# Kernel optimization log

Hardware: AMD Instinct MI355X
Metric: run time of the kernel (lower is better)

Reference implementation:

```python
import jax, jax.numpy as jnp
import numpy as np


def _hann_filter(P):
    # ramp filter built in spatial domain (Kak & Slaney) times fftshifted Hann window
    n = np.concatenate([np.arange(1, P // 2 + 1, 2), np.arange(P // 2 - 1, 0, -2)]).astype(np.float64)
    f = np.zeros(P, np.float64)
    f[0] = 0.25
    f[1::2] = -1.0 / (np.pi * n) ** 2
    ramp = 2.0 * np.real(np.fft.fft(f))
    filt = ramp * np.fft.fftshift(np.hanning(P))
    return jnp.asarray(filt, jnp.float32)


def _fbp(sino, angles, circle):
    B, A, L = sino.shape
    P = max(64, int(2 ** np.ceil(np.log2(2 * L))))  # img_size_padded
    center = L // 2
    # --- FFT filtering (filtered=True) ---
    filt = _hann_filter(P)
    sino_p = jnp.pad(sino, ((0, 0), (0, 0), (0, P - L)))
    sino_f = jnp.real(jnp.fft.ifft(jnp.fft.fft(sino_p, axis=-1) * filt, axis=-1))[:, :, :L]
    # --- back-projection: emulate grid_sample(bilinear, align_corners=True, padding zeros) ---
    x, y = jnp.meshgrid(jnp.arange(L, dtype=jnp.float32) - center,
                        jnp.arange(L, dtype=jnp.float32) - center, indexing='ij')
    th = angles + jnp.pi / 2
    t = x[None] * jnp.cos(th)[:, None, None] + y[None] * jnp.sin(th)[:, None, None]  # [A,L,L]
    # t_norm = 2t/(L-1); align_corners pixel coord = (t_norm+1)/2*(L-1) = t + (L-1)/2
    u = t + (L - 1) / 2.0
    i0 = jnp.floor(u)
    frac = u - i0
    i0i = i0.astype(jnp.int32)
    i1i = i0i + 1
    v0 = (i0i >= 0) & (i0i < L)
    v1 = (i1i >= 0) & (i1i < L)
    w0 = jnp.where(v0, 1.0 - frac, 0.0)  # zero-padding: kill OOB taps
    w1 = jnp.where(v1, frac, 0.0)
    aidx = jnp.arange(A)[:, None, None]
    g0 = sino_f[:, aidx, jnp.clip(i0i, 0, L - 1)]  # [B,A,L,L]
    g1 = sino_f[:, aidx, jnp.clip(i1i, 0, L - 1)]
    recon = jnp.sum(w0[None] * g0 + w1[None] * g1, axis=1)  # [B,L,L]
    if circle:
        Y, X = np.ogrid[:L, :L]
        mask = jnp.asarray(np.sqrt((X - center) ** 2 + (Y - center) ** 2) > center)
        recon = jnp.where(mask[None], 0.0, recon)
    return recon


def setup_inputs() -> dict:
    key = jax.random.key(0)
    sino = jax.random.normal(key, (2, 181, 512), dtype=jnp.float32)
    angles = jnp.linspace(0.0, np.pi, 181).astype(jnp.float32)
    return {"sino": sino, "angles": angles, "circle": 1}


def reference(sino, angles, circle):
    return _fbp(sino, angles, circle)
```

## Files before the change

### kernel.cpp

```cpp
#include <hip/hip_runtime.h>
#include <math.h>

#define OFF_FILT 0
#define OFF_HR   1024
#define OFF_CTH  2048
#define OFF_STH  2304
#define OFF_SF   4096

__device__ __forceinline__ float cos2pi(float x) {
  return __builtin_amdgcn_cosf(x);
}

__global__ __launch_bounds__(256) void k_filt(const float* __restrict__ angles,
                                              float* __restrict__ ws,
                                              float* __restrict__ out) {
  const int t = threadIdx.x & 63;
  const int k = blockIdx.x * 4 + (threadIdx.x >> 6);
  float acc = 0.f;
#pragma unroll
  for (int q = 0; q < 8; q++) {
    int tt = t + 64 * q;
    int n = (tt < 256) ? (2 * tt + 1) : (1023 - 2 * tt);
    float pin = 3.14159265358979f * (float)n;
    float cf = -1.0f / (pin * pin);
    int r = ((2 * tt + 1) * k) & 1023;
    acc = fmaf(cf, cos2pi((float)r * (1.0f / 1024.0f)), acc);
  }
#pragma unroll
  for (int o = 32; o; o >>= 1) acc += __shfl_down(acc, o, 64);
  if (t == 0) {
    float ramp = 0.5f + 2.0f * acc;
    int ks = (k + 512) & 1023;
    float hann = 0.5f - 0.5f * cos2pi((float)ks * (1.0f / 1023.0f));
    ws[OFF_FILT + k] = ramp * hann;
  }
  if (blockIdx.x == 0 && threadIdx.x < 181) {
    float th = angles[threadIdx.x] + 1.5707963267948966f;
    ws[OFF_CTH + threadIdx.x] = cosf(th);
    ws[OFF_STH + threadIdx.x] = sinf(th);
  }
  const float4 z4 = make_float4(0.f, 0.f, 0.f, 0.f);
  float4* o4 = (float4*)out;
  int idx = blockIdx.x * 256 + threadIdx.x;
  o4[idx] = z4;
  o4[idx + 65536] = z4;
}

__global__ __launch_bounds__(256) void k_hr(float* __restrict__ ws) {
  const int t = threadIdx.x & 63;
  const int m = blockIdx.x * 4 + (threadIdx.x >> 6);
  float acc = 0.f;
  int r = (t * m) & 1023;
  const int step = (64 * m) & 1023;
#pragma unroll
  for (int q = 0; q < 16; q++) {
    acc = fmaf(ws[OFF_FILT + t + 64 * q],
               cos2pi((float)r * (1.0f / 1024.0f)), acc);
    r = (r + step) & 1023;
  }
#pragma unroll
  for (int o = 32; o; o >>= 1) acc += __shfl_down(acc, o, 64);
  if (t == 0) ws[OFF_HR + m] = acc * (1.0f / 1024.0f);
}

__global__ __launch_bounds__(64) void k_conv(const float* __restrict__ sino,
                                             float* __restrict__ ws) {
  __shared__ float s_s0[512];
  __shared__ float s_s1[512];
  __shared__ float s_hr[1024];
  const int t = threadIdx.x;
  const int a = blockIdx.x;
  const float4* r0 = (const float4*)(sino + (size_t)a * 512);
  const float4* r1 = (const float4*)(sino + (size_t)(181 + a) * 512);
  ((float4*)s_s0)[t] = r0[t];
  ((float4*)s_s0)[t + 64] = r0[t + 64];
  ((float4*)s_s1)[t] = r1[t];
  ((float4*)s_s1)[t + 64] = r1[t + 64];
  const float4* hr4 = (const float4*)(ws + OFF_HR);
#pragma unroll
  for (int q = 0; q < 4; q++) ((float4*)s_hr)[t + 64 * q] = hr4[t + 64 * q];
  __syncthreads();

  const int base = blockIdx.y * 256 + t * 4;
  float acc0[4] = {0.f, 0.f, 0.f, 0.f};
  float acc1[4] = {0.f, 0.f, 0.f, 0.f};
  const float4* SH = (const float4*)s_hr;
  const float4* S0 = (const float4*)s_s0;
  const float4* S1 = (const float4*)s_s1;
  for (int j8 = 0; j8 < 512; j8 += 8) {
    float4 sa0 = S0[j8 >> 2];
    float4 sb0 = S0[(j8 >> 2) + 1];
    float4 sa1 = S1[j8 >> 2];
    float4 sb1 = S1[(j8 >> 2) + 1];
    int w = base - j8;
    float4 h0 = SH[((w - 8) & 1023) >> 2];
    float4 h1 = SH[((w - 4) & 1023) >> 2];
    float4 h2 = SH[(w & 1023) >> 2];
    float qq[12] = {h0.x, h0.y, h0.z, h0.w, h1.x, h1.y,
                    h1.z, h1.w, h2.x, h2.y, h2.z, h2.w};
    float v0[8] = {sa0.x, sa0.y, sa0.z, sa0.w, sb0.x, sb0.y, sb0.z, sb0.w};
    float v1[8] = {sa1.x, sa1.y, sa1.z, sa1.w, sb1.x, sb1.y, sb1.z, sb1.w};
#pragma unroll
    for (int jj = 0; jj < 8; jj++) {
#pragma unroll
      for (int m = 0; m < 4; m++) {
        acc0[m] = fmaf(v0[jj], qq[8 + m - jj], acc0[m]);
        acc1[m] = fmaf(v1[jj], qq[8 + m - jj], acc1[m]);
      }
    }
  }
  float* dst = ws + OFF_SF + (size_t)a * 1024 + base * 2;
  ((float4*)dst)[0] = make_float4(acc0[0], acc1[0], acc0[1], acc1[1]);
  ((float4*)dst)[1] = make_float4(acc0[2], acc1[2], acc0[3], acc1[3]);
}

#define PAD   108
#define ROWE  728
#define CHUNK 4
__global__ __launch_bounds__(512) void k_bp(const float* __restrict__ ws,
                                            const int* __restrict__ circ,
                                            float* __restrict__ out) {
  __shared__ float2 srow[CHUNK * ROWE];
  const int j = threadIdx.x;
  const int i = blockIdx.x;
  const int abase = blockIdx.y * 91;
  const int acnt = min(91, 181 - abase);
  const float xc = (float)(i - 256);
  const float yc = (float)(j - 256);
  const float* __restrict__ cth = ws + OFF_CTH;
  const float* __restrict__ sth = ws + OFF_STH;
  float acc0 = 0.f, acc1 = 0.f;

  const float2 z2 = make_float2(0.f, 0.f);
#pragma unroll
  for (int r = 0; r < CHUNK; r++) {
    if (j < PAD) srow[r * ROWE + j] = z2;
    if (j < ROWE - PAD - 512) srow[r * ROWE + PAD + 512 + j] = z2;
  }

  const int r0 = j >> 8, r1 = r0 + 2;
  const int p0 = (j & 255) * 2;
  const int col = j & 255;
  const float4* __restrict__ G = (const float4*)(ws + OFF_SF);
  float4* SW0 = (float4*)&srow[r0 * ROWE + PAD + p0];
  float4* SW1 = (float4*)&srow[r1 * ROWE + PAD + p0];
  const int rowcap = abase + acnt - 1;

  int A = abase;
  float4 pre0 = G[min(A + r0, rowcap) * 256 + col];
  float4 pre1 = G[min(A + r1, rowcap) * 256 + col];

  for (int c = 0; c < 23; c++) {
    __syncthreads();
    *SW0 = pre0;
    *SW1 = pre1;
    const int An = A + CHUNK;
    if (c < 22) {
      pre0 = G[min(An + r0, rowcap) * 256 + col];
      pre1 = G[min(An + r1, rowcap) * 256 + col];
    }
    __syncthreads();
    const int nv = min(CHUNK, abase + acnt - A);
#pragma unroll
    for (int r = 0; r < CHUNK; r++) {
      if (r >= nv) break;
      const int a = A + r;
      const float c_ = cth[a];
      const float s_ = sth[a];
      float u = fmaf(xc, c_, fmaf(yc, s_, 255.5f + (float)PAD));
      float fl = floorf(u);
      float fr = u - fl;
      int b = (int)fl;
      const float2* rp = &srow[r * ROWE];
      float2 t0 = rp[b];
      float2 t1 = rp[b + 1];
      float w0 = 1.0f - fr;
      acc0 = fmaf(w0, t0.x, fmaf(fr, t1.x, acc0));
      acc1 = fmaf(w0, t0.y, fmaf(fr, t1.y, acc1));
    }
    A = An;
  }
  const int dx = j - 256, dy = i - 256;
  const bool msk = (circ[0] != 0) && (dx * dx + dy * dy > 65536);
  if (!msk) {
    const size_t o = (size_t)i * 512 + j;
    atomicAdd(&out[o], acc0);
    atomicAdd(&out[262144 + o], acc1);
  }
}

extern "C" void kernel_launch(void* const* d_in, const int* in_sizes, int n_in,
                              void* d_out, int out_size, void* d_ws, size_t ws_size,
                              hipStream_t stream) {
  const float* sino = (const float*)d_in[0];
  const float* angles = (const float*)d_in[1];
  const int* circ = (const int*)d_in[2];
  float* ws = (float*)d_ws;
  float* out = (float*)d_out;

  hipLaunchKernelGGL(k_filt, dim3(256),    dim3(256), 0, stream, angles, ws, out);
  hipLaunchKernelGGL(k_hr,   dim3(256),    dim3(256), 0, stream, ws);
  hipLaunchKernelGGL(k_conv, dim3(181, 2), dim3(64),  0, stream, sino, ws);
  hipLaunchKernelGGL(k_bp,   dim3(512, 2), dim3(512), 0, stream, ws, circ, out);
}
```

Baseline: 96.53 us.

## Fuse all FBP stages into one cooperative persistent kernel with grid syncs

Replaces the four separate launches (filter build, impulse response, convolution, back-projection) with a single cooperative kernel of 512 blocks that separates the phases with grid.sync(). The convolution is split across 8 wavefronts per block with a shared-memory reduction. The back-projection now processes all 181 angles per row block, so the output is written directly and no longer zeroed and accumulated with atomics. This removes launch gaps and atomics, but it relies on all 512 blocks being co-resident, pays for grid-wide barriers, and halves the number of back-projection blocks. The old four-kernel path is kept as a fallback if the cooperative launch fails.

```diff
diff --git a/kernel.cpp b/kernel.cpp
--- a/kernel.cpp
+++ b/kernel.cpp
@@ -1,5 +1,8 @@
 #include <hip/hip_runtime.h>
+#include <hip/hip_cooperative_groups.h>
 #include <math.h>
+
+namespace cg = cooperative_groups;
 
 #define OFF_FILT 0
 #define OFF_HR   1024
@@ -7,8 +10,194 @@
 #define OFF_STH  2304
 #define OFF_SF   4096
 
+#define PAD   108
+#define ROWE  728
+#define CHUNK 4
+
 __device__ __forceinline__ float cos2pi(float x) {
   return __builtin_amdgcn_cosf(x);
+}
+
+__global__ __launch_bounds__(512, 4) void k_fused(const float* __restrict__ sino,
+                                                  const float* __restrict__ angles,
+                                                  const int* __restrict__ circ,
+                                                  float* __restrict__ ws,
+                                                  float* __restrict__ out) {
+  cg::grid_group grid = cg::this_grid();
+  __shared__ float smem[6144];
+  const int tid = threadIdx.x;
+  const int bid = blockIdx.x;
+  const int lane = tid & 63;
+
+  if (tid < 128) {
+    const int k = bid * 2 + (tid >> 6);
+    float acc = 0.f;
+#pragma unroll
+    for (int q = 0; q < 8; q++) {
+      int tt = lane + 64 * q;
+      int n = (tt < 256) ? (2 * tt + 1) : (1023 - 2 * tt);
+      float pin = 3.14159265358979f * (float)n;
+      float cf = -1.0f / (pin * pin);
+      int r = ((2 * tt + 1) * k) & 1023;
+      acc = fmaf(cf, cos2pi((float)r * (1.0f / 1024.0f)), acc);
+    }
+#pragma unroll
+    for (int o = 32; o; o >>= 1) acc += __shfl_down(acc, o, 64);
+    if (lane == 0) {
+      float ramp = 0.5f + 2.0f * acc;
+      int ks = (k + 512) & 1023;
+      float hann = 0.5f - 0.5f * cos2pi((float)ks * (1.0f / 1023.0f));
+      ws[OFF_FILT + k] = ramp * hann;
+    }
+  } else if (bid == 0 && tid < 309) {
+    int a = tid - 128;
+    float th = angles[a] + 1.5707963267948966f;
+    ws[OFF_CTH + a] = cosf(th);
+    ws[OFF_STH + a] = sinf(th);
+  }
+  grid.sync();
+
+  if (tid < 128) {
+    const int m = bid * 2 + (tid >> 6);
+    float acc = 0.f;
+    int r = (lane * m) & 1023;
+    const int step = (64 * m) & 1023;
+#pragma unroll
+    for (int q = 0; q < 16; q++) {
+      acc = fmaf(ws[OFF_FILT + lane + 64 * q],
+                 cos2pi((float)r * (1.0f / 1024.0f)), acc);
+      r = (r + step) & 1023;
+    }
+#pragma unroll
+    for (int o = 32; o; o >>= 1) acc += __shfl_down(acc, o, 64);
+    if (lane == 0) ws[OFF_HR + m] = acc * (1.0f / 1024.0f);
+  }
+  grid.sync();
+
+  if (bid < 362) {
+    const int a = bid >> 1;
+    const int half = bid & 1;
+    float* s_s0 = smem;
+    float* s_s1 = smem + 512;
+    float* s_hr = smem + 1024;
+    float* part = smem + 2048;
+    if (tid < 128) {
+      ((float4*)s_s0)[tid] = ((const float4*)(sino + (size_t)a * 512))[tid];
+    } else if (tid < 256) {
+      ((float4*)s_s1)[tid - 128] =
+          ((const float4*)(sino + (size_t)(181 + a) * 512))[tid - 128];
+    } else {
+      ((float4*)s_hr)[tid - 256] = ((const float4*)(ws + OFF_HR))[tid - 256];
+    }
+    __syncthreads();
+
+    const int w = tid >> 6;
+    const int base = half * 256 + lane * 4;
+    float acc0[4] = {0.f, 0.f, 0.f, 0.f};
+    float acc1[4] = {0.f, 0.f, 0.f, 0.f};
+    const float4* SH = (const float4*)s_hr;
+    const float4* S0 = (const float4*)s_s0;
+    const float4* S1 = (const float4*)s_s1;
+#pragma unroll
+    for (int ii = 0; ii < 8; ii++) {
+      const int j8 = w * 64 + ii * 8;
+      float4 sa0 = S0[j8 >> 2];
+      float4 sb0 = S0[(j8 >> 2) + 1];
+      float4 sa1 = S1[j8 >> 2];
+      float4 sb1 = S1[(j8 >> 2) + 1];
+      int wi = base - j8;
+      float4 h0 = SH[((wi - 8) & 1023) >> 2];
+      float4 h1 = SH[((wi - 4) & 1023) >> 2];
+      float4 h2 = SH[(wi & 1023) >> 2];
+      float qq[12] = {h0.x, h0.y, h0.z, h0.w, h1.x, h1.y,
+                      h1.z, h1.w, h2.x, h2.y, h2.z, h2.w};
+      float v0[8] = {sa0.x, sa0.y, sa0.z, sa0.w, sb0.x, sb0.y, sb0.z, sb0.w};
+      float v1[8] = {sa1.x, sa1.y, sa1.z, sa1.w, sb1.x, sb1.y, sb1.z, sb1.w};
+#pragma unroll
+      for (int jj = 0; jj < 8; jj++) {
+#pragma unroll
+        for (int m = 0; m < 4; m++) {
+          acc0[m] = fmaf(v0[jj], qq[8 + m - jj], acc0[m]);
+          acc1[m] = fmaf(v1[jj], qq[8 + m - jj], acc1[m]);
+        }
+      }
+    }
+    float* pw = part + w * 512 + lane * 8;
+    ((float4*)pw)[0] = make_float4(acc0[0], acc1[0], acc0[1], acc1[1]);
+    ((float4*)pw)[1] = make_float4(acc0[2], acc1[2], acc0[3], acc1[3]);
+    __syncthreads();
+    float s = part[tid];
+#pragma unroll
+    for (int ww = 1; ww < 8; ww++) s += part[ww * 512 + tid];
+    ws[OFF_SF + (size_t)a * 1024 + half * 512 + tid] = s;
+  }
+  grid.sync();
+
+  {
+    float2* srow = (float2*)smem;
+    const int j = tid;
+    const int i = bid;
+    const float xc = (float)(i - 256);
+    const float yc = (float)(j - 256);
+    const float* __restrict__ cth = ws + OFF_CTH;
+    const float* __restrict__ sth = ws + OFF_STH;
+    float acc0 = 0.f, acc1 = 0.f;
+
+    const float2 z2 = make_float2(0.f, 0.f);
+#pragma unroll
+    for (int r = 0; r < CHUNK; r++) {
+      if (j < PAD) srow[r * ROWE + j] = z2;
+      if (j < ROWE - PAD - 512) srow[r * ROWE + PAD + 512 + j] = z2;
+    }
+
+    const int r0 = j >> 8, r1 = r0 + 2;
+    const int p0 = (j & 255) * 2;
+    const int col = j & 255;
+    const float4* __restrict__ G = (const float4*)(ws + OFF_SF);
+    float4* SW0 = (float4*)&srow[r0 * ROWE + PAD + p0];
+    float4* SW1 = (float4*)&srow[r1 * ROWE + PAD + p0];
+    const int rowcap = 180;
+
+    int A = 0;
+    float4 pre0 = G[min(r0, rowcap) * 256 + col];
+    float4 pre1 = G[min(r1, rowcap) * 256 + col];
+
+    for (int c = 0; c < 46; c++) {
+      __syncthreads();
+      *SW0 = pre0;
+      *SW1 = pre1;
+      const int An = A + CHUNK;
+      if (c < 45) {
+        pre0 = G[min(An + r0, rowcap) * 256 + col];
+        pre1 = G[min(An + r1, rowcap) * 256 + col];
+      }
+      __syncthreads();
+      const int nv = min(CHUNK, 181 - A);
+#pragma unroll
+      for (int r = 0; r < CHUNK; r++) {
+        if (r >= nv) break;
+        const int a = A + r;
+        const float c_ = cth[a];
+        const float s_ = sth[a];
+        float u = fmaf(xc, c_, fmaf(yc, s_, 255.5f + (float)PAD));
+        float fl = floorf(u);
+        float fr = u - fl;
+        int b = (int)fl;
+        const float2* rp = &srow[r * ROWE];
+        float2 t0 = rp[b];
+        float2 t1 = rp[b + 1];
+        float w0 = 1.0f - fr;
+        acc0 = fmaf(w0, t0.x, fmaf(fr, t1.x, acc0));
+        acc1 = fmaf(w0, t0.y, fmaf(fr, t1.y, acc1));
+      }
+      A = An;
+    }
+    const int dx = j - 256, dy = i - 256;
+    const bool msk = (circ[0] != 0) && (dx * dx + dy * dy > 65536);
+    const size_t o = (size_t)i * 512 + j;
+    out[o] = msk ? 0.f : acc0;
+    out[262144 + o] = msk ? 0.f : acc1;
+  }
 }
 
 __global__ __launch_bounds__(256) void k_filt(const float* __restrict__ angles,
@@ -114,9 +303,6 @@
   ((float4*)dst)[1] = make_float4(acc0[2], acc1[2], acc0[3], acc1[3]);
 }
 
-#define PAD   108
-#define ROWE  728
-#define CHUNK 4
 __global__ __launch_bounds__(512) void k_bp(const float* __restrict__ ws,
                                             const int* __restrict__ circ,
                                             float* __restrict__ out) {
@@ -198,8 +384,14 @@
   float* ws = (float*)d_ws;
   float* out = (float*)d_out;
 
-  hipLaunchKernelGGL(k_filt, dim3(256),    dim3(256), 0, stream, angles, ws, out);
-  hipLaunchKernelGGL(k_hr,   dim3(256),    dim3(256), 0, stream, ws);
-  hipLaunchKernelGGL(k_conv, dim3(181, 2), dim3(64),  0, stream, sino, ws);
-  hipLaunchKernelGGL(k_bp,   dim3(512, 2), dim3(512), 0, stream, ws, circ, out);
-}
+  void* args[] = {(void*)&sino, (void*)&angles, (void*)&circ, (void*)&ws, (void*)&out};
+  hipError_t e = hipLaunchCooperativeKernel(reinterpret_cast<void*>(k_fused),
+                                            dim3(512), dim3(512), args, 0, stream);
+  if (e != hipSuccess) {
+    (void)hipGetLastError();
+    hipLaunchKernelGGL(k_filt, dim3(256),    dim3(256), 0, stream, angles, ws, out);
+    hipLaunchKernelGGL(k_hr,   dim3(256),    dim3(256), 0, stream, ws);
+    hipLaunchKernelGGL(k_conv, dim3(181, 2), dim3(64),  0, stream, sino, ws);
+    hipLaunchKernelGGL(k_bp,   dim3(512, 2), dim3(512), 0, stream, ws, circ, out);
+  }
+}
```

After: 259.8 us. +169.1%, slower.

## Split convolution across 8 waves and drop angle split with atomics in backprojection

Applied to the files above, without the earlier changes.

The convolution kernel now uses 512 threads per block, with each wave handling a 64-sample slice of the input and partial sums reduced through shared memory. This raises parallelism over the previous single-wave blocks. The backprojection no longer splits angles across two blocks. Each block loops over all 181 angles and writes its output directly, so the output zeroing pass and the atomic adds are removed. The catch is half as many backprojection blocks, each with twice the serial work, plus a cheaper truncation in place of floor, which relies on the coordinate being non-negative thanks to the padding.

```diff
diff --git a/kernel.cpp b/kernel.cpp
--- a/kernel.cpp
+++ b/kernel.cpp
@@ -7,13 +7,16 @@
 #define OFF_STH  2304
 #define OFF_SF   4096
 
+#define PAD   108
+#define ROWE  728
+#define CHUNK 4
+
 __device__ __forceinline__ float cos2pi(float x) {
   return __builtin_amdgcn_cosf(x);
 }
 
 __global__ __launch_bounds__(256) void k_filt(const float* __restrict__ angles,
-                                              float* __restrict__ ws,
-                                              float* __restrict__ out) {
+                                              float* __restrict__ ws) {
   const int t = threadIdx.x & 63;
   const int k = blockIdx.x * 4 + (threadIdx.x >> 6);
   float acc = 0.f;
@@ -39,11 +42,6 @@
     ws[OFF_CTH + threadIdx.x] = cosf(th);
     ws[OFF_STH + threadIdx.x] = sinf(th);
   }
-  const float4 z4 = make_float4(0.f, 0.f, 0.f, 0.f);
-  float4* o4 = (float4*)out;
-  int idx = blockIdx.x * 256 + threadIdx.x;
-  o4[idx] = z4;
-  o4[idx + 65536] = z4;
 }
 
 __global__ __launch_bounds__(256) void k_hr(float* __restrict__ ws) {
@@ -63,39 +61,45 @@
   if (t == 0) ws[OFF_HR + m] = acc * (1.0f / 1024.0f);
 }
 
-__global__ __launch_bounds__(64) void k_conv(const float* __restrict__ sino,
-                                             float* __restrict__ ws) {
-  __shared__ float s_s0[512];
-  __shared__ float s_s1[512];
-  __shared__ float s_hr[1024];
-  const int t = threadIdx.x;
-  const int a = blockIdx.x;
-  const float4* r0 = (const float4*)(sino + (size_t)a * 512);
-  const float4* r1 = (const float4*)(sino + (size_t)(181 + a) * 512);
-  ((float4*)s_s0)[t] = r0[t];
-  ((float4*)s_s0)[t + 64] = r0[t + 64];
-  ((float4*)s_s1)[t] = r1[t];
-  ((float4*)s_s1)[t + 64] = r1[t + 64];
-  const float4* hr4 = (const float4*)(ws + OFF_HR);
-#pragma unroll
-  for (int q = 0; q < 4; q++) ((float4*)s_hr)[t + 64 * q] = hr4[t + 64 * q];
+__global__ __launch_bounds__(512) void k_conv(const float* __restrict__ sino,
+                                              float* __restrict__ ws) {
+  __shared__ float smem[6144];
+  const int tid = threadIdx.x;
+  const int a = blockIdx.x >> 1;
+  const int half = blockIdx.x & 1;
+  const int lane = tid & 63;
+  float* s_s0 = smem;
+  float* s_s1 = smem + 512;
+  float* s_hr = smem + 1024;
+  float* part = smem + 2048;
+  if (tid < 128) {
+    ((float4*)s_s0)[tid] = ((const float4*)(sino + (size_t)a * 512))[tid];
+  } else if (tid < 256) {
+    ((float4*)s_s1)[tid - 128] =
+        ((const float4*)(sino + (size_t)(181 + a) * 512))[tid - 128];
+  } else {
+    ((float4*)s_hr)[tid - 256] = ((const float4*)(ws + OFF_HR))[tid - 256];
+  }
   __syncthreads();
 
-  const int base = blockIdx.y * 256 + t * 4;
+  const int w = tid >> 6;
+  const int base = half * 256 + lane * 4;
   float acc0[4] = {0.f, 0.f, 0.f, 0.f};
   float acc1[4] = {0.f, 0.f, 0.f, 0.f};
   const float4* SH = (const float4*)s_hr;
   const float4* S0 = (const float4*)s_s0;
   const float4* S1 = (const float4*)s_s1;
-  for (int j8 = 0; j8 < 512; j8 += 8) {
+#pragma unroll
+  for (int ii = 0; ii < 8; ii++) {
+    const int j8 = w * 64 + ii * 8;
     float4 sa0 = S0[j8 >> 2];
     float4 sb0 = S0[(j8 >> 2) + 1];
     float4 sa1 = S1[j8 >> 2];
     float4 sb1 = S1[(j8 >> 2) + 1];
-    int w = base - j8;
-    float4 h0 = SH[((w - 8) & 1023) >> 2];
-    float4 h1 = SH[((w - 4) & 1023) >> 2];
-    float4 h2 = SH[(w & 1023) >> 2];
+    int wi = base - j8;
+    float4 h0 = SH[((wi - 8) & 1023) >> 2];
+    float4 h1 = SH[((wi - 4) & 1023) >> 2];
+    float4 h2 = SH[(wi & 1023) >> 2];
     float qq[12] = {h0.x, h0.y, h0.z, h0.w, h1.x, h1.y,
                     h1.z, h1.w, h2.x, h2.y, h2.z, h2.w};
     float v0[8] = {sa0.x, sa0.y, sa0.z, sa0.w, sb0.x, sb0.y, sb0.z, sb0.w};
@@ -109,22 +113,22 @@
       }
     }
   }
-  float* dst = ws + OFF_SF + (size_t)a * 1024 + base * 2;
-  ((float4*)dst)[0] = make_float4(acc0[0], acc1[0], acc0[1], acc1[1]);
-  ((float4*)dst)[1] = make_float4(acc0[2], acc1[2], acc0[3], acc1[3]);
-}
-
-#define PAD   108
-#define ROWE  728
-#define CHUNK 4
+  float* pw = part + w * 512 + lane * 8;
+  ((float4*)pw)[0] = make_float4(acc0[0], acc1[0], acc0[1], acc1[1]);
+  ((float4*)pw)[1] = make_float4(acc0[2], acc1[2], acc0[3], acc1[3]);
+  __syncthreads();
+  float s = part[tid];
+#pragma unroll
+  for (int ww = 1; ww < 8; ww++) s += part[ww * 512 + tid];
+  ws[OFF_SF + (size_t)a * 1024 + half * 512 + tid] = s;
+}
+
 __global__ __launch_bounds__(512) void k_bp(const float* __restrict__ ws,
                                             const int* __restrict__ circ,
                                             float* __restrict__ out) {
   __shared__ float2 srow[CHUNK * ROWE];
   const int j = threadIdx.x;
   const int i = blockIdx.x;
-  const int abase = blockIdx.y * 91;
-  const int acnt = min(91, 181 - abase);
   const float xc = (float)(i - 256);
   const float yc = (float)(j - 256);
   const float* __restrict__ cth = ws + OFF_CTH;
@@ -144,23 +148,23 @@
   const float4* __restrict__ G = (const float4*)(ws + OFF_SF);
   float4* SW0 = (float4*)&srow[r0 * ROWE + PAD + p0];
   float4* SW1 = (float4*)&srow[r1 * ROWE + PAD + p0];
-  const int rowcap = abase + acnt - 1;
-
-  int A = abase;
-  float4 pre0 = G[min(A + r0, rowcap) * 256 + col];
-  float4 pre1 = G[min(A + r1, rowcap) * 256 + col];
-
-  for (int c = 0; c < 23; c++) {
+  const int rowcap = 180;
+
+  int A = 0;
+  float4 pre0 = G[min(r0, rowcap) * 256 + col];
+  float4 pre1 = G[min(r1, rowcap) * 256 + col];
+
+  for (int c = 0; c < 46; c++) {
     __syncthreads();
     *SW0 = pre0;
     *SW1 = pre1;
     const int An = A + CHUNK;
-    if (c < 22) {
+    if (c < 45) {
       pre0 = G[min(An + r0, rowcap) * 256 + col];
       pre1 = G[min(An + r1, rowcap) * 256 + col];
     }
     __syncthreads();
-    const int nv = min(CHUNK, abase + acnt - A);
+    const int nv = min(CHUNK, 181 - A);
 #pragma unroll
     for (int r = 0; r < CHUNK; r++) {
       if (r >= nv) break;
@@ -168,9 +172,8 @@
       const float c_ = cth[a];
       const float s_ = sth[a];
       float u = fmaf(xc, c_, fmaf(yc, s_, 255.5f + (float)PAD));
-      float fl = floorf(u);
-      float fr = u - fl;
-      int b = (int)fl;
+      int b = (int)u;
+      float fr = u - (float)b;
       const float2* rp = &srow[r * ROWE];
       float2 t0 = rp[b];
       float2 t1 = rp[b + 1];
@@ -182,11 +185,9 @@
   }
   const int dx = j - 256, dy = i - 256;
   const bool msk = (circ[0] != 0) && (dx * dx + dy * dy > 65536);
-  if (!msk) {
-    const size_t o = (size_t)i * 512 + j;
-    atomicAdd(&out[o], acc0);
-    atomicAdd(&out[262144 + o], acc1);
-  }
+  const size_t o = (size_t)i * 512 + j;
+  out[o] = msk ? 0.f : acc0;
+  out[262144 + o] = msk ? 0.f : acc1;
 }
 
 extern "C" void kernel_launch(void* const* d_in, const int* in_sizes, int n_in,
@@ -198,8 +199,8 @@
   float* ws = (float*)d_ws;
   float* out = (float*)d_out;
 
-  hipLaunchKernelGGL(k_filt, dim3(256),    dim3(256), 0, stream, angles, ws, out);
-  hipLaunchKernelGGL(k_hr,   dim3(256),    dim3(256), 0, stream, ws);
-  hipLaunchKernelGGL(k_conv, dim3(181, 2), dim3(64),  0, stream, sino, ws);
-  hipLaunchKernelGGL(k_bp,   dim3(512, 2), dim3(512), 0, stream, ws, circ, out);
-}
+  hipLaunchKernelGGL(k_filt, dim3(256), dim3(256), 0, stream, angles, ws);
+  hipLaunchKernelGGL(k_hr,   dim3(256), dim3(256), 0, stream, ws);
+  hipLaunchKernelGGL(k_conv, dim3(362), dim3(512), 0, stream, sino, ws);
+  hipLaunchKernelGGL(k_bp,   dim3(512), dim3(512), 0, stream, ws, circ, out);
+}
```

Measured after the change: 94.68 us. No clear change (-1.9%).
